# Kernel optimization log

Measured on AMD Instinct MI355X. Metric: run time of the kernel, lower is better.

Reference implementation:

```python
import jax, jax.numpy as jnp
import numpy as np

B, S, E, H = 2, 2048, 1024, 16
D = E // H  # head dimension = 64


def setup_inputs() -> dict:
    key = jax.random.key(0)
    ks = jax.random.split(key, 12)
    scale_in = 1.0 / np.sqrt(E)
    x = jax.random.normal(ks[0], (B, S, E), dtype=jnp.float32)
    # random 0/1 attention mask (1 = attend, 0 = masked out)
    mask = jax.random.randint(ks[1], (B, S, S), 0, 2, dtype=jnp.int32)
    # per-head QKV projections, stacked over the head axis: [H, E, D]
    Wq = jax.random.normal(ks[2], (H, E, D), dtype=jnp.float32) * scale_in
    bq = jnp.zeros((H, D), dtype=jnp.float32)
    Wk = jax.random.normal(ks[3], (H, E, D), dtype=jnp.float32) * scale_in
    bk = jnp.zeros((H, D), dtype=jnp.float32)
    Wv = jax.random.normal(ks[4], (H, E, D), dtype=jnp.float32) * scale_in
    bv = jnp.zeros((H, D), dtype=jnp.float32)
    # output projection: [H*D, E] == [E, E]
    Wo = jax.random.normal(ks[5], (H * D, E), dtype=jnp.float32) * scale_in
    bo = jnp.zeros((E,), dtype=jnp.float32)
    return {"x": x, "mask": mask, "Wq": Wq, "bq": bq, "Wk": Wk, "bk": bk,
            "Wv": Wv, "bv": bv, "Wo": Wo, "bo": bo}


def reference(x, mask, Wq, bq, Wk, bk, Wv, bv, Wo, bo):
    # Batched equivalent of the per-head Python loop: all heads at once.
    q = jnp.einsum('bse,hed->bhsd', x, Wq) + bq[None, :, None, :]  # [B,H,S,D]
    k = jnp.einsum('bse,hed->bhsd', x, Wk) + bk[None, :, None, :]
    v = jnp.einsum('bse,hed->bhsd', x, Wv) + bv[None, :, None, :]
    scale = 1.0 / jnp.sqrt(jnp.asarray(D, dtype=q.dtype))
    scores = jnp.einsum('bhsd,bhtd->bhst', q, k) * scale          # [B,H,S,S]
    scores = jnp.where(mask[:, None, :, :] != 0, scores, jnp.asarray(-1e9, scores.dtype))
    attn = jax.nn.softmax(scores, axis=-1)
    ctx = jnp.einsum('bhst,bhtd->bhsd', attn, v)                  # [B,H,S,D]
    # concat heads along feature dim (torch.cat(dim=2))
    concat = jnp.transpose(ctx, (0, 2, 1, 3)).reshape(B, S, H * D)
    return concat @ Wo + bo
```

## Files before the change

kernel.cpp:

```cpp
#include <hip/hip_runtime.h>

#define S_LEN 2048
#define EMB   1024
#define NH    16
#define HD    64
#define BS    2
#define QSCALE 0.18033688f

typedef __bf16 bf16;
typedef bf16  bf16x8 __attribute__((ext_vector_type(8)));
typedef bf16  bf16x4 __attribute__((ext_vector_type(4)));
typedef float f32x4  __attribute__((ext_vector_type(4)));
typedef unsigned long long u64;
typedef unsigned int u32;

__device__ __forceinline__ bf16x8 ld8(const bf16* p){ return *(const bf16x8*)p; }

__device__ __forceinline__ void gl_lds16(const bf16* g, void* l) {
    __builtin_amdgcn_global_load_lds(
        (const __attribute__((address_space(1))) void*)g,
        (__attribute__((address_space(3))) void*)l,
        16, 0, 0);
}

#define SW(row, g) ((((g) ^ ((row) & 7))) * 8)

__global__ __launch_bounds__(256)
void pack_mask(const int* __restrict__ mask, u64* __restrict__ pm)
{
    int lane = threadIdx.x & 63;
    int row  = blockIdx.x * 4 + (threadIdx.x >> 6);
    const int* mr = mask + (size_t)row * S_LEN;
    u64* pr = pm + (size_t)row * (S_LEN / 64);
    for (int i = 0; i < S_LEN / 64; ++i) {
        u64 bits = __ballot(mr[i * 64 + lane] != 0);
        if (lane == 0) pr[i] = bits;
    }
}

__global__ __launch_bounds__(256)
void prep(const float* __restrict__ x, bf16* __restrict__ xbf,
          const int* __restrict__ mask, u64* __restrict__ pm,
          const float* __restrict__ W0, const float* __restrict__ W1,
          const float* __restrict__ W2, const float* __restrict__ W3,
          bf16* __restrict__ Wt)
{
    const int bid = blockIdx.x;
    const int tid = threadIdx.x;
    __shared__ float T[64][68];

    if (bid < 1024) {
        size_t i = ((size_t)bid * 256 + tid) * 16;
        bf16 t[16];
        #pragma unroll
        for (int g = 0; g < 4; ++g) {
            f32x4 v = *(const f32x4*)(x + i + g * 4);
            #pragma unroll
            for (int j = 0; j < 4; ++j) t[g * 4 + j] = (bf16)v[j];
        }
        *(bf16x8*)(xbf + i)     = *(bf16x8*)t;
        *(bf16x8*)(xbf + i + 8) = *(bf16x8*)(t + 8);
    } else if (bid < 2048) {
        int lane = tid & 63;
        int row  = (bid - 1024) * 4 + (tid >> 6);
        const int* mr = mask + (size_t)row * S_LEN;
        u64* pr = pm + (size_t)row * (S_LEN / 64);
        for (int i = 0; i < S_LEN / 64; ++i) {
            u64 bits = __ballot(mr[i * 64 + lane] != 0);
            if (lane == 0) pr[i] = bits;
        }
    } else {
        const int t   = bid - 2048;
        const int z   = t >> 8;
        const int rem = t & 255;
        const int k0 = (rem & 15) * 64, n0 = (rem >> 4) * 64;
        const float* W = z == 0 ? W0 : z == 1 ? W1 : z == 2 ? W2 : W3;
        const bool head = z < 3;
        {
            int k = k0 + (tid >> 2), cg = (tid & 3) * 16;
            size_t base = head ? ((size_t)(n0 >> 6) * ((size_t)EMB * HD) + (size_t)k * HD + cg)
                               : ((size_t)k * EMB + n0 + cg);
            #pragma unroll
            for (int g = 0; g < 4; ++g) {
                f32x4 v = *(const f32x4*)(W + base + g * 4);
                #pragma unroll
                for (int j = 0; j < 4; ++j) T[tid >> 2][cg + g * 4 + j] = v[j];
            }
        }
        __syncthreads();
        {
            int n = n0 + (tid >> 2), ck = (tid & 3) * 16;
            bf16 t16[16];
            #pragma unroll
            for (int j = 0; j < 16; ++j) t16[j] = (bf16)T[ck + j][tid >> 2];
            bf16* outp = Wt + (size_t)z * EMB * EMB + (size_t)n * EMB + k0 + ck;
            *(bf16x8*)outp       = *(bf16x8*)t16;
            *(bf16x8*)(outp + 8) = *(bf16x8*)(t16 + 8);
        }
    }
}

__global__ __launch_bounds__(256)
void scale_q(bf16* __restrict__ q)
{
    size_t i = ((size_t)blockIdx.x * 256 + threadIdx.x) * 8;
    bf16x8 v = *(bf16x8*)(q + i);
    #pragma unroll
    for (int j = 0; j < 8; ++j) v[j] = (bf16)((float)v[j] * QSCALE);
    *(bf16x8*)(q + i) = v;
}

__global__ __launch_bounds__(256, 3)
void gemm_qkv(const void* __restrict__ Ap, const bf16* __restrict__ Wt,
              const float* __restrict__ bqp, const float* __restrict__ bkp,
              const float* __restrict__ bvp,
              bf16* __restrict__ qb, bf16* __restrict__ kb, bf16* __restrict__ VT,
              int a32)
{
    const int tid  = threadIdx.x;
    const int lane = tid & 63, quad = lane >> 4, c = lane & 15;
    const int w = tid >> 6, wm = w >> 1, wn = w & 1;
    const int flat = blockIdx.y * 32 + blockIdx.x;
    const int xcd = flat & 7, li = flat >> 3;
    const int m0 = ((xcd >> 1) * 8 + (li & 7)) * 128;
    const int n0 = ((xcd & 1) * 12 + (li >> 3)) * 128;

    __shared__ bf16 Ash[128][64];
    __shared__ bf16 Wsh[128][64];
    __shared__ bf16 Ush[4][16][72];

    f32x4 acc[4][4];
    #pragma unroll
    for (int mt = 0; mt < 4; ++mt)
        #pragma unroll
        for (int nt = 0; nt < 4; ++nt) acc[mt][nt] = (f32x4){0.f,0.f,0.f,0.f};

    const int lrow = lane >> 3, lcol = (lane & 7) * 8;

    for (int k0 = 0; k0 < EMB; k0 += 64) {
        __syncthreads();
        if (!a32) {
            const bf16* A = (const bf16*)Ap;
            #pragma unroll
            for (int j = 0; j < 4; ++j)
                gl_lds16(A + (size_t)(m0 + w * 32 + j * 8 + lrow) * EMB + k0 + lcol,
                         &Ash[w * 32 + j * 8][0]);
        } else {
            const float* A = (const float*)Ap + (size_t)(m0 + (tid >> 1)) * EMB + k0 + (tid & 1) * 32;
            bf16 t[32];
            #pragma unroll
            for (int g = 0; g < 8; ++g) {
                f32x4 v = *(const f32x4*)(A + g * 4);
                #pragma unroll
                for (int j = 0; j < 4; ++j) t[g * 4 + j] = (bf16)v[j];
            }
            #pragma unroll
            for (int g2 = 0; g2 < 4; ++g2)
                *(bf16x8*)&Ash[tid >> 1][(tid & 1) * 32 + g2 * 8] = *(bf16x8*)(t + g2 * 8);
        }
        #pragma unroll
        for (int j = 0; j < 4; ++j)
            gl_lds16(Wt + (size_t)(n0 + w * 32 + j * 8 + lrow) * EMB + k0 + lcol,
                     &Wsh[w * 32 + j * 8][0]);
        __syncthreads();

        #pragma unroll
        for (int kh = 0; kh < 2; ++kh) {
            bf16x8 af[4], bfv[4];
            #pragma unroll
            for (int mt = 0; mt < 4; ++mt) af[mt]  = ld8(&Ash[wm * 64 + mt * 16 + c][kh * 32 + quad * 8]);
            #pragma unroll
            for (int nt = 0; nt < 4; ++nt) bfv[nt] = ld8(&Wsh[wn * 64 + nt * 16 + c][kh * 32 + quad * 8]);
            #pragma unroll
            for (int mt = 0; mt < 4; ++mt)
                #pragma unroll
                for (int nt = 0; nt < 4; ++nt)
                    acc[mt][nt] = __builtin_amdgcn_mfma_f32_16x16x32_bf16(af[mt], bfv[nt], acc[mt][nt], 0, 0, 0);
        }
    }

    const int z = n0 >> 10;
    const float* bias = z == 0 ? bqp : z == 1 ? bkp : bvp;
    if (z == 2) {
        #pragma unroll
        for (int nt = 0; nt < 4; ++nt) {
            int nn = (n0 & 1023) + wn * 64 + nt * 16 + c;
            float bv_ = bias[nn];
            int head = nn >> 6, d = nn & 63;
            #pragma unroll
            for (int mt = 0; mt < 4; ++mt) {
                int m = m0 + wm * 64 + mt * 16 + quad * 4;
                bf16x4 pv;
                #pragma unroll
                for (int r = 0; r < 4; ++r) pv[r] = (bf16)(acc[mt][nt][r] + bv_);
                *(bf16x4*)&VT[((size_t)((m >> 11) * NH + head) * HD + d) * S_LEN + (m & 2047)] = pv;
            }
        }
    } else {
        bf16* outb = z == 0 ? qb : kb;
        const float scl = z == 0 ? QSCALE : 1.0f;
        float bv4[4];
        #pragma unroll
        for (int nt = 0; nt < 4; ++nt) bv4[nt] = bias[(n0 & 1023) + wn * 64 + nt * 16 + c];
        #pragma unroll
        for (int mt = 0; mt < 4; ++mt) {
            #pragma unroll
            for (int nt = 0; nt < 4; ++nt)
                #pragma unroll
                for (int r = 0; r < 4; ++r)
                    Ush[w][quad * 4 + r][nt * 16 + c] = (bf16)((acc[mt][nt][r] + bv4[nt]) * scl);
            __builtin_amdgcn_s_waitcnt(0xc07f);
            int row16 = lane >> 2, cg = (lane & 3) * 16;
            int m = m0 + wm * 64 + mt * 16 + row16;
            int nn0 = (n0 & 1023) + wn * 64 + cg;
            bf16x8 v0 = *(bf16x8*)&Ush[w][row16][cg];
            bf16x8 v1 = *(bf16x8*)&Ush[w][row16][cg + 8];
            *(bf16x8*)&outb[(size_t)m * EMB + nn0]     = v0;
            *(bf16x8*)&outb[(size_t)m * EMB + nn0 + 8] = v1;
            __builtin_amdgcn_s_waitcnt(0xc07f);
        }
    }
}

__global__ __launch_bounds__(256, 4)
void gemm_o(const bf16* __restrict__ Ap, const bf16* __restrict__ Wt,
            const float* __restrict__ bo, float* __restrict__ C)
{
    const int tid  = threadIdx.x;
    const int lane = tid & 63, quad = lane >> 4, c = lane & 15;
    const int w = tid >> 6, wm = w >> 1, wn = w & 1;
    const int flat = blockIdx.y * 32 + blockIdx.x;
    const int xcd = flat & 7, li = flat >> 3;
    const int m0 = ((xcd >> 1) * 8 + (li & 7)) * 128;
    const int n0 = ((xcd & 1) * 8 + (li >> 3)) * 64;

    __shared__ bf16 Ash[128][64];
    __shared__ bf16 Wsh[64][64];

    f32x4 acc[4][2];
    #pragma unroll
    for (int mt = 0; mt < 4; ++mt)
        #pragma unroll
        for (int nt = 0; nt < 2; ++nt) acc[mt][nt] = (f32x4){0.f,0.f,0.f,0.f};

    const int lrow = lane >> 3, lcol = (lane & 7) * 8;

    for (int k0 = 0; k0 < EMB; k0 += 64) {
        __syncthreads();
        #pragma unroll
        for (int j = 0; j < 4; ++j)
            gl_lds16(Ap + (size_t)(m0 + w * 32 + j * 8 + lrow) * EMB + k0 + lcol,
                     &Ash[w * 32 + j * 8][0]);
        #pragma unroll
        for (int j = 0; j < 2; ++j)
            gl_lds16(Wt + (size_t)(n0 + w * 16 + j * 8 + lrow) * EMB + k0 + lcol,
                     &Wsh[w * 16 + j * 8][0]);
        __syncthreads();

        #pragma unroll
        for (int kh = 0; kh < 2; ++kh) {
            bf16x8 af[4], bfv[2];
            #pragma unroll
            for (int mt = 0; mt < 4; ++mt) af[mt]  = ld8(&Ash[wm * 64 + mt * 16 + c][kh * 32 + quad * 8]);
            #pragma unroll
            for (int nt = 0; nt < 2; ++nt) bfv[nt] = ld8(&Wsh[wn * 32 + nt * 16 + c][kh * 32 + quad * 8]);
            #pragma unroll
            for (int mt = 0; mt < 4; ++mt)
                #pragma unroll
                for (int nt = 0; nt < 2; ++nt)
                    acc[mt][nt] = __builtin_amdgcn_mfma_f32_16x16x32_bf16(af[mt], bfv[nt], acc[mt][nt], 0, 0, 0);
        }
    }

    __syncthreads();
    float (*Ush)[16][36] = (float(*)[16][36])&Ash[0][0];
    float bv2[2];
    #pragma unroll
    for (int nt = 0; nt < 2; ++nt) bv2[nt] = bo[n0 + wn * 32 + nt * 16 + c];
    #pragma unroll
    for (int mt = 0; mt < 4; ++mt) {
        #pragma unroll
        for (int nt = 0; nt < 2; ++nt)
            #pragma unroll
            for (int r = 0; r < 4; ++r)
                Ush[w][quad * 4 + r][nt * 16 + c] = acc[mt][nt][r] + bv2[nt];
        __builtin_amdgcn_s_waitcnt(0xc07f);
        int row16 = lane >> 2, cg = (lane & 3) * 8;
        int m = m0 + wm * 64 + mt * 16 + row16;
        int nn = n0 + wn * 32 + cg;
        f32x4 v0 = *(f32x4*)&Ush[w][row16][cg];
        f32x4 v1 = *(f32x4*)&Ush[w][row16][cg + 4];
        *(f32x4*)&C[(size_t)m * EMB + nn]     = v0;
        *(f32x4*)&C[(size_t)m * EMB + nn + 4] = v1;
        __builtin_amdgcn_s_waitcnt(0xc07f);
    }
}

__global__ __launch_bounds__(512)
void gemm128(const void* __restrict__ Ap, const float* __restrict__ Wp,
             const bf16* __restrict__ Wtp, const float* __restrict__ bias,
             void* __restrict__ Cp, int N, int K, int whead,
             int m_base, int a32, int cmode)
{
    const int tid  = threadIdx.x;
    const int lane = tid & 63, quad = lane >> 4, c = lane & 15;
    const int w = tid >> 6, wm = w >> 2, wn = w & 3;
    const int m0 = blockIdx.x * 128, n0 = blockIdx.y * 128;

    __shared__ bf16 Ash[128][64];
    __shared__ bf16 Wsh[128][64];

    f32x4 acc[4][2];
    #pragma unroll
    for (int mt = 0; mt < 4; ++mt)
        #pragma unroll
        for (int nt = 0; nt < 2; ++nt) acc[mt][nt] = (f32x4){0.f,0.f,0.f,0.f};

    const int arow = tid >> 2, aq = tid & 3;

    auto compute = [&]() {
        #pragma unroll
        for (int kh = 0; kh < 2; ++kh) {
            bf16x8 bfr[2];
            #pragma unroll
            for (int nt = 0; nt < 2; ++nt) {
                int rw = wn * 32 + nt * 16 + c;
                bfr[nt] = ld8(&Wsh[rw][SW(rw, kh * 4 + quad)]);
            }
            #pragma unroll
            for (int mt = 0; mt < 4; ++mt) {
                int ra = wm * 64 + mt * 16 + c;
                bf16x8 af = ld8(&Ash[ra][SW(ra, kh * 4 + quad)]);
                #pragma unroll
                for (int nt = 0; nt < 2; ++nt)
                    acc[mt][nt] = __builtin_amdgcn_mfma_f32_16x16x32_bf16(af, bfr[nt], acc[mt][nt], 0, 0, 0);
            }
        }
    };

    for (int k0 = 0; k0 < K; k0 += 64) {
        __syncthreads();
        if (a32) {
            const float* A = (const float*)Ap + (size_t)(m_base + m0 + arow) * K + k0 + aq * 16;
            bf16 t16[16];
            #pragma unroll
            for (int g = 0; g < 4; ++g) {
                f32x4 v = *(const f32x4*)(A + g * 4);
                #pragma unroll
                for (int j = 0; j < 4; ++j) t16[g * 4 + j] = (bf16)v[j];
            }
            *(bf16x8*)&Ash[arow][SW(arow, aq * 2)]     = *(bf16x8*)t16;
            *(bf16x8*)&Ash[arow][SW(arow, aq * 2 + 1)] = *(bf16x8*)(t16 + 8);
        } else {
            const bf16* A = (const bf16*)Ap + (size_t)(m_base + m0 + arow) * K + k0 + aq * 16;
            *(bf16x8*)&Ash[arow][SW(arow, aq * 2)]     = ld8(A);
            *(bf16x8*)&Ash[arow][SW(arow, aq * 2 + 1)] = ld8(A + 8);
        }
        {
            int nl = tid & 127, kg = tid >> 7;
            int n = n0 + nl;
            size_t base    = whead ? ((size_t)(n >> 6) * ((size_t)K * HD) + (n & 63))
                                   : (size_t)n;
            size_t kstride = whead ? (size_t)HD : (size_t)N;
            #pragma unroll
            for (int p = 0; p < 2; ++p) {
                int grp = kg + 4 * p;
                bf16 t8[8];
                #pragma unroll
                for (int j = 0; j < 8; ++j)
                    t8[j] = (bf16)Wp[base + (size_t)(k0 + grp * 8 + j) * kstride];
                *(bf16x8*)&Wsh[nl][SW(nl, grp)] = *(bf16x8*)t8;
            }
        }
        __syncthreads();
        compute();
    }

    #pragma unroll
    for (int nt = 0; nt < 2; ++nt) {
        int n = n0 + wn * 32 + nt * 16 + c;
        float bv_ = bias[n];
        #pragma unroll
        for (int mt = 0; mt < 4; ++mt)
            #pragma unroll
            for (int r = 0; r < 4; ++r) {
                int m = m0 + wm * 64 + mt * 16 + quad * 4 + r;
                float v = acc[mt][nt][r] + bv_;
                if (cmode == 0)      ((bf16*)Cp)[(size_t)m * N + n] = (bf16)v;
                else if (cmode == 1) ((float*)Cp)[(size_t)m * N + n] = v;
                else {
                    int mm = m_base + m;
                    ((bf16*)Cp)[((size_t)((mm >> 11) * NH + (n >> 6)) * HD + (n & 63)) * S_LEN + (mm & 2047)] = (bf16)v;
                }
            }
    }
}

__global__ __launch_bounds__(512, 2)
void attn_kernel(bf16* q0p, bf16* q1p, const bf16* __restrict__ kbuf,
                 const bf16* __restrict__ VTg, const u64* __restrict__ pmask)
{
    const int tid  = threadIdx.x;
    const int w    = tid >> 6;
    const int lane = tid & 63;
    const int quad = lane >> 4;
    const int c    = lane & 15;
    const int flat  = blockIdx.y * 16 + blockIdx.x;
    const int flat2 = (flat & 7) * 64 + (flat >> 3);
    const int q0   = (flat2 & 15) * 128;
    const int bh   = flat2 >> 4;
    const int b    = bh >> 4, h = bh & 15;

    bf16* qc = b ? q1p : q0p;
    const bf16* kh_ = kbuf + (size_t)b * S_LEN * EMB + h * HD;
    const bf16* vt  = VTg + (size_t)bh * HD * S_LEN;

    __shared__ bf16 Ksh [2][64][64];
    __shared__ bf16 VTsh[2][64][64];
    __shared__ bf16 Psh[8][16][64];

    bf16x8 qf[2];
    #pragma unroll
    for (int kk = 0; kk < 2; ++kk)
        qf[kk] = ld8(qc + (size_t)(q0 + w * 16 + c) * EMB + h * HD + kk * 32 + quad * 8);

    const u64* pmr = pmask + (size_t)(b * S_LEN + q0 + w * 16 + c) * (S_LEN / 64);

    f32x4 l4 = (f32x4){0.f,0.f,0.f,0.f};
    f32x4 o[4];
    #pragma unroll
    for (int dt = 0; dt < 4; ++dt) o[dt] = (f32x4){0.f,0.f,0.f,0.f};

    const int srow = tid >> 3, sg = tid & 7;
    bf16x8 kr, vr;
    auto loadKV = [&](int t0) {
        kr = ld8(kh_ + (size_t)(t0 + srow) * EMB + sg * 8);
        vr = ld8(vt + (size_t)srow * S_LEN + t0 + sg * 8);
    };

    loadKV(0);
    int buf = 0;
    for (int t0 = 0; t0 < S_LEN; t0 += 64) {
        *(bf16x8*)&Ksh [buf][srow][SW(srow, sg)] = kr;
        *(bf16x8*)&VTsh[buf][srow][SW(srow, sg)] = vr;
        __syncthreads();
        if (t0 + 64 < S_LEN) loadKV(t0 + 64);

        u64 s0 = pmr[t0 >> 6] >> (quad * 4);
        u32 mm[2] = {(u32)s0, (u32)(s0 >> 32)};

        f32x4 sc[4];
        #pragma unroll
        for (int tt = 0; tt < 4; ++tt) sc[tt] = (f32x4){0.f,0.f,0.f,0.f};
        #pragma unroll
        for (int tt = 0; tt < 4; ++tt)
            #pragma unroll
            for (int kk = 0; kk < 2; ++kk) {
                int rk = tt * 16 + c;
                bf16x8 ka = ld8(&Ksh[buf][rk][SW(rk, kk * 4 + quad)]);
                sc[tt] = __builtin_amdgcn_mfma_f32_16x16x32_bf16(ka, qf[kk], sc[tt], 0, 0, 0);
            }

        #pragma unroll
        for (int tt = 0; tt < 4; ++tt) {
            u32 half = mm[tt >> 1];
            bf16x4 pv;
            #pragma unroll
            for (int r = 0; r < 4; ++r) {
                float e = __builtin_amdgcn_exp2f(sc[tt][r]);
                e = ((half >> ((tt & 1) * 16 + r)) & 1) ? e : 0.f;
                l4[r] += e;
                pv[r] = (bf16)e;
            }
            *(bf16x4*)&Psh[w][c][SW(c, tt * 2 + (quad >> 1)) + (quad & 1) * 4] = pv;
        }
        __builtin_amdgcn_s_waitcnt(0xc07f);

        #pragma unroll
        for (int th = 0; th < 2; ++th) {
            bf16x8 pf = ld8(&Psh[w][c][SW(c, th * 4 + quad)]);
            #pragma unroll
            for (int dt = 0; dt < 4; ++dt) {
                int rv = dt * 16 + c;
                bf16x8 av = ld8(&VTsh[buf][rv][SW(rv, th * 4 + quad)]);
                o[dt] = __builtin_amdgcn_mfma_f32_16x16x32_bf16(av, pf, o[dt], 0, 0, 0);
            }
        }
        buf ^= 1;
    }

    float ls = l4[0] + l4[1] + l4[2] + l4[3];
    ls += __shfl_xor(ls, 16);
    ls += __shfl_xor(ls, 32);
    float inv = 1.0f / fmaxf(ls, 1e-30f);
    #pragma unroll
    for (int dt = 0; dt < 4; ++dt) {
        bf16x4 ov;
        #pragma unroll
        for (int r = 0; r < 4; ++r) ov[r] = (bf16)(o[dt][r] * inv);
        *(bf16x4*)&qc[(size_t)(q0 + w * 16 + c) * EMB + h * HD + dt * 16 + quad * 4] = ov;
    }
}

extern "C" void kernel_launch(void* const* d_in, const int* in_sizes, int n_in,
                              void* d_out, int out_size, void* d_ws, size_t ws_size,
                              hipStream_t stream)
{
    const float* x    = (const float*)d_in[0];
    const int*   mask = (const int*)d_in[1];
    const float* Wq   = (const float*)d_in[2];
    const float* bq   = (const float*)d_in[3];
    const float* Wk   = (const float*)d_in[4];
    const float* bk   = (const float*)d_in[5];
    const float* Wv   = (const float*)d_in[6];
    const float* bv   = (const float*)d_in[7];
    const float* Wo   = (const float*)d_in[8];
    const float* bo   = (const float*)d_in[9];
    float* out = (float*)d_out;

    const size_t SLAB = (size_t)S_LEN * EMB;
    const size_t QB = (size_t)BS * SLAB * sizeof(bf16);
    const size_t WT = (size_t)4 * EMB * EMB * sizeof(bf16);
    const size_t PM = (size_t)BS * S_LEN * (S_LEN / 64) * 8;
    const size_t XB = (size_t)BS * SLAB * sizeof(bf16);

    bf16* VT = (bf16*)d_out;
    bf16* kb = (bf16*)d_out + BS * SLAB;

    dim3 b256(256), b512(512);
    dim3 gAtt (S_LEN / 128, BS * NH);
    dim3 gPk  (BS * S_LEN / 4);
    dim3 gFull(BS * S_LEN / 128, EMB / 128);
    dim3 gHalf(S_LEN / 128, EMB / 128);

    if (ws_size >= QB + WT + PM + XB + 64) {
        bf16* qb  = (bf16*)d_ws;
        bf16* Wt  = (bf16*)((char*)d_ws + QB);
        u64*  pm  = (u64*)((char*)d_ws + QB + WT);
        bf16* xbf = (bf16*)((char*)d_ws + QB + WT + PM);

        prep<<<dim3(3072), b256, 0, stream>>>(x, xbf, mask, pm, Wq, Wk, Wv, Wo, Wt);

        gemm_qkv<<<dim3(BS * S_LEN / 128, 3 * EMB / 128), b256, 0, stream>>>(
            xbf, Wt, bq, bk, bv, qb, kb, VT, 0);

        attn_kernel<<<gAtt, b512, 0, stream>>>(qb, qb + SLAB, kb, VT, pm);

        gemm_o<<<dim3(BS * S_LEN / 128, EMB / 64), b256, 0, stream>>>(
            qb, Wt + (size_t)3 * EMB * EMB, bo, out);
    } else if (ws_size >= QB + PM + 64) {
        bf16* qb = (bf16*)d_ws;
        u64*  pm = (u64*)((char*)d_ws + QB);
        pack_mask<<<gPk, b256, 0, stream>>>(mask, pm);

        gemm128<<<gFull, b512, 0, stream>>>(x, Wk, nullptr, bk, kb, EMB, EMB, 1, 0, 1, 0);
        gemm128<<<gFull, b512, 0, stream>>>(x, Wv, nullptr, bv, VT, EMB, EMB, 1, 0, 1, 2);
        gemm128<<<gFull, b512, 0, stream>>>(x, Wq, nullptr, bq, qb, EMB, EMB, 1, 0, 1, 0);
        scale_q<<<dim3(BS * SLAB / (256 * 8)), b256, 0, stream>>>(qb);

        attn_kernel<<<gAtt, b512, 0, stream>>>(qb, qb + SLAB, kb, VT, pm);

        gemm128<<<gFull, b512, 0, stream>>>(qb, Wo, nullptr, bo, out, EMB, EMB, 0, 0, 0, 1);
    } else {
        bf16* qb0 = (bf16*)d_in[4];
        bf16* qb1 = (bf16*)d_in[6];
        u64*  pm  = (u64*)d_in[2];

        gemm128<<<gFull, b512, 0, stream>>>(x, Wk, nullptr, bk, kb, EMB, EMB, 1, 0, 1, 0);
        gemm128<<<gFull, b512, 0, stream>>>(x, Wv, nullptr, bv, VT, EMB, EMB, 1, 0, 1, 2);
        gemm128<<<gHalf, b512, 0, stream>>>(x, Wq, nullptr, bq, qb0, EMB, EMB, 1, 0,     1, 0);
        gemm128<<<gHalf, b512, 0, stream>>>(x, Wq, nullptr, bq, qb1, EMB, EMB, 1, S_LEN, 1, 0);
        scale_q<<<dim3(SLAB / (256 * 8)), b256, 0, stream>>>(qb0);
        scale_q<<<dim3(SLAB / (256 * 8)), b256, 0, stream>>>(qb1);
        pack_mask<<<gPk, b256, 0, stream>>>(mask, pm);

        attn_kernel<<<gAtt, b512, 0, stream>>>(qb0, qb1, kb, VT, pm);

        gemm128<<<gHalf, b512, 0, stream>>>(qb0, Wo, nullptr, bo, out,        EMB, EMB, 0, 0, 0, 1);
        gemm128<<<gHalf, b512, 0, stream>>>(qb1, Wo, nullptr, bo, out + SLAB, EMB, EMB, 0, 0, 0, 1);
    }
}
```

Measured before the change: 232.3 us.

## Load K fragments directly from global and raise occupancy in attention and QKV GEMM

The attention kernel no longer stages K tiles through LDS. Each wave loads its K MFMA fragments straight from global memory (L2-cached) inside the loop. The QKV GEMM epilogue reuses the A tile's shared memory instead of a separate buffer. Both kernels raise their launch_bounds occupancy targets. This cuts LDS footprint and traffic so more blocks fit per CU, but K loads are now uncoalesced, redundant across waves, issued without prefetch, and may stall the MFMA chain.

Result: slower. 334.7 us (+44.0%).

```diff
diff --git a/kernel.cpp b/kernel.cpp
--- a/kernel.cpp
+++ b/kernel.cpp
@@ -110,7 +110,7 @@
     *(bf16x8*)(q + i) = v;
 }
 
-__global__ __launch_bounds__(256, 3)
+__global__ __launch_bounds__(256, 4)
 void gemm_qkv(const void* __restrict__ Ap, const bf16* __restrict__ Wt,
               const float* __restrict__ bqp, const float* __restrict__ bkp,
               const float* __restrict__ bvp,
@@ -127,7 +127,6 @@
 
     __shared__ bf16 Ash[128][64];
     __shared__ bf16 Wsh[128][64];
-    __shared__ bf16 Ush[4][16][72];
 
     f32x4 acc[4][4];
     #pragma unroll
@@ -197,6 +196,8 @@
             }
         }
     } else {
+        __syncthreads();
+        bf16 (*Ush)[16][72] = (bf16 (*)[16][72])&Ash[0][0];
         bf16* outb = z == 0 ? qb : kb;
         const float scl = z == 0 ? QSCALE : 1.0f;
         float bv4[4];
@@ -396,7 +397,7 @@
     }
 }
 
-__global__ __launch_bounds__(512, 2)
+__global__ __launch_bounds__(512, 4)
 void attn_kernel(bf16* q0p, bf16* q1p, const bf16* __restrict__ kbuf,
                  const bf16* __restrict__ VTg, const u64* __restrict__ pmask)
 {
@@ -415,7 +416,6 @@
     const bf16* kh_ = kbuf + (size_t)b * S_LEN * EMB + h * HD;
     const bf16* vt  = VTg + (size_t)bh * HD * S_LEN;
 
-    __shared__ bf16 Ksh [2][64][64];
     __shared__ bf16 VTsh[2][64][64];
     __shared__ bf16 Psh[8][16][64];
 
@@ -431,20 +431,29 @@
     #pragma unroll
     for (int dt = 0; dt < 4; ++dt) o[dt] = (f32x4){0.f,0.f,0.f,0.f};
 
+    bf16x8 kf[4][2];
+    const bf16* kfb = kh_ + (size_t)c * EMB + quad * 8;
+    auto loadK = [&](int t0) {
+        #pragma unroll
+        for (int tt = 0; tt < 4; ++tt)
+            #pragma unroll
+            for (int kk = 0; kk < 2; ++kk)
+                kf[tt][kk] = ld8(kfb + (size_t)(t0 + tt * 16) * EMB + kk * 32);
+    };
+
     const int srow = tid >> 3, sg = tid & 7;
-    bf16x8 kr, vr;
-    auto loadKV = [&](int t0) {
-        kr = ld8(kh_ + (size_t)(t0 + srow) * EMB + sg * 8);
+    bf16x8 vr;
+    auto loadV = [&](int t0) {
         vr = ld8(vt + (size_t)srow * S_LEN + t0 + sg * 8);
     };
 
-    loadKV(0);
+    loadV(0);
     int buf = 0;
     for (int t0 = 0; t0 < S_LEN; t0 += 64) {
-        *(bf16x8*)&Ksh [buf][srow][SW(srow, sg)] = kr;
         *(bf16x8*)&VTsh[buf][srow][SW(srow, sg)] = vr;
         __syncthreads();
-        if (t0 + 64 < S_LEN) loadKV(t0 + 64);
+        if (t0 + 64 < S_LEN) loadV(t0 + 64);
+        loadK(t0);
 
         u64 s0 = pmr[t0 >> 6] >> (quad * 4);
         u32 mm[2] = {(u32)s0, (u32)(s0 >> 32)};
@@ -455,11 +464,8 @@
         #pragma unroll
         for (int tt = 0; tt < 4; ++tt)
             #pragma unroll
-            for (int kk = 0; kk < 2; ++kk) {
-                int rk = tt * 16 + c;
-                bf16x8 ka = ld8(&Ksh[buf][rk][SW(rk, kk * 4 + quad)]);
-                sc[tt] = __builtin_amdgcn_mfma_f32_16x16x32_bf16(ka, qf[kk], sc[tt], 0, 0, 0);
-            }
+            for (int kk = 0; kk < 2; ++kk)
+                sc[tt] = __builtin_amdgcn_mfma_f32_16x16x32_bf16(kf[tt][kk], qf[kk], sc[tt], 0, 0, 0);
 
         #pragma unroll
         for (int tt = 0; tt < 4; ++tt) {
```
